# Kernel optimization log

Hardware: AMD Instinct MI355X
Metric: run time of the kernel (lower is better)

The kernel has to match this reference:

```python
import jax, jax.numpy as jnp
import numpy as np

V, D, H, L, F, S, B = 32000, 1024, 16, 6, 4096, 1024, 2
DK = D // H
SCALE = float(np.sqrt(DK))
NEG = -1e9


def _make_pe(max_len, d_model):
    pos = np.arange(max_len, dtype=np.float32)[:, None]
    div = np.exp(np.arange(0, d_model, 2, dtype=np.float32) * (-np.log(10000.0) / d_model))
    pe = np.zeros((max_len, d_model), dtype=np.float32)
    pe[:, 0::2] = np.sin(pos * div)
    pe[:, 1::2] = np.cos(pos * div)
    return jnp.asarray(pe)


def _ln(x, g, b, eps=1e-5):
    m = x.mean(-1, keepdims=True)
    v = ((x - m) ** 2).mean(-1, keepdims=True)
    return (x - m) / jnp.sqrt(v + eps) * g + b


def setup_inputs() -> dict:
    key = jax.random.key(0)
    ks = jax.random.split(key, 10)
    std = 0.02
    tokens = jax.random.randint(ks[0], (B, S), 0, V)
    emb = (jax.random.normal(ks[1], (V, D)) * std).at[0].set(0.0)  # padding_idx=0 row zeroed
    pe = _make_pe(4096, D)
    Wq = jax.random.normal(ks[2], (L, D, D)) * std
    Wk = jax.random.normal(ks[3], (L, D, D)) * std
    Wv = jax.random.normal(ks[4], (L, D, D)) * std
    Wo = jax.random.normal(ks[5], (L, D, D)) * std
    bo = jnp.zeros((L, D))
    g1 = jnp.ones((L, D)); be1 = jnp.zeros((L, D))
    g2 = jnp.ones((L, D)); be2 = jnp.zeros((L, D))
    W1 = jax.random.normal(ks[6], (L, D, F)) * std
    b1 = jnp.zeros((L, F))
    W2 = jax.random.normal(ks[7], (L, F, D)) * std
    b2 = jnp.zeros((L, D))
    gf = jnp.ones((D,)); bf = jnp.zeros((D,))
    Wout = jax.random.normal(ks[8], (D, V)) * std
    bout = jnp.zeros((V,))
    return dict(tokens=tokens, emb=emb, pe=pe, Wq=Wq, Wk=Wk, Wv=Wv, Wo=Wo, bo=bo,
                g1=g1, be1=be1, g2=g2, be2=be2, W1=W1, b1=b1, W2=W2, b2=b2,
                gf=gf, bf=bf, Wout=Wout, bout=bout)


def reference(tokens, emb, pe, Wq, Wk, Wv, Wo, bo, g1, be1, g2, be2,
              W1, b1, W2, b2, gf, bf, Wout, bout):
    Bx, Sx = tokens.shape
    x = emb[tokens] * jnp.sqrt(jnp.float32(D)) + pe[:Sx]  # (B,S,D)
    pad = tokens == 0  # (B,S) padding mask
    causal = jnp.triu(jnp.ones((Sx, Sx), dtype=bool), 1)
    mask = causal[None, None] | pad[:, None, None, :]  # (B,1,S,S), True = masked
    for l in range(L):
        h = _ln(x, g1[l], be1[l])
        q = (h @ Wq[l]).reshape(Bx, Sx, H, DK)
        k = (h @ Wk[l]).reshape(Bx, Sx, H, DK)
        v = (h @ Wv[l]).reshape(Bx, Sx, H, DK)
        scores = jnp.einsum('bqhd,bkhd->bhqk', q, k) / SCALE
        scores = jnp.where(mask, NEG, scores)  # masked_fill(mask, -1e9)
        a = jax.nn.softmax(scores, axis=-1)
        ctx = jnp.einsum('bhqk,bkhd->bqhd', a, v).reshape(Bx, Sx, D)
        x = x + ctx @ Wo[l] + bo[l]
        h = _ln(x, g2[l], be2[l])
        x = x + jax.nn.gelu(h @ W1[l] + b1[l], approximate=False) @ W2[l] + b2[l]
    x = _ln(x, gf, bf)
    return x @ Wout + bout  # (B,S,V)
```

## Files before the change

### kernel.cpp

```cpp
#include <hip/hip_runtime.h>
#include <hip/hip_bf16.h>
#include <stdint.h>

typedef __hip_bfloat16 bf16;
typedef __attribute__((ext_vector_type(8))) short bf16x8;
typedef __attribute__((ext_vector_type(4))) float f32x4;

#define DEV static __device__ __forceinline__

DEV float b2f(bf16 v) { return __bfloat162float(v); }
DEV bf16  f2b(float v) { return __float2bfloat16(v); }

DEV float u2f(unsigned short u) {
  unsigned int x = (unsigned int)u << 16;
  float f;
  __builtin_memcpy(&f, &x, 4);
  return f;
}

DEV void gload16(const void* g, void* l) {
  __builtin_amdgcn_global_load_lds(
      (__attribute__((address_space(1))) void*)(void*)g,
      (__attribute__((address_space(3))) void*)l, 16, 0, 0);
}

DEV f32x4 mfma16(bf16x8 a, bf16x8 b, f32x4 c) {
  return __builtin_amdgcn_mfma_f32_16x16x32_bf16(a, b, c, 0, 0, 0);
}

__global__ __launch_bounds__(256) void embed_kernel(
    const int* __restrict__ tok, const float* __restrict__ emb,
    const float* __restrict__ pe, float* __restrict__ x)
{
  const int r = blockIdx.x, t = threadIdx.x;
  const int s = r & 1023;
  const int tk = tok[r];
  const int d = t * 4;
  const float* ep = emb + (size_t)tk * 1024 + d;
  const float* pp = pe + (size_t)s * 1024 + d;
  float* xp = x + (size_t)r * 1024 + d;
  #pragma unroll
  for (int j = 0; j < 4; ++j)
    xp[j] = ep[j] * 32.0f + pp[j];
}

__global__ __launch_bounds__(256) void ln_kernel(
    const float* __restrict__ x, const float* __restrict__ g,
    const float* __restrict__ be, bf16* __restrict__ h)
{
  const int r = blockIdx.x, t = threadIdx.x;
  const float4 v = ((const float4*)(x + (size_t)r * 1024))[t];
  float s  = v.x + v.y + v.z + v.w;
  float sq = v.x * v.x + v.y * v.y + v.z * v.z + v.w * v.w;
  #pragma unroll
  for (int d = 1; d < 64; d <<= 1) {
    s  += __shfl_xor(s, d);
    sq += __shfl_xor(sq, d);
  }
  __shared__ float red[8];
  const int w = t >> 6, l = t & 63;
  if (l == 0) { red[w] = s; red[4 + w] = sq; }
  __syncthreads();
  s  = red[0] + red[1] + red[2] + red[3];
  sq = red[4] + red[5] + red[6] + red[7];
  const float mean = s * (1.0f / 1024.0f);
  const float var  = sq * (1.0f / 1024.0f) - mean * mean;
  const float inv  = 1.0f / sqrtf(var + 1e-5f);
  bf16* hp = h + (size_t)r * 1024 + t * 4;
  const float* gp = g + t * 4;
  const float* bp = be + t * 4;
  const float vv[4] = {v.x, v.y, v.z, v.w};
  #pragma unroll
  for (int j = 0; j < 4; ++j)
    hp[j] = f2b((vv[j] - mean) * inv * gp[j] + bp[j]);
}

__global__ __launch_bounds__(256) void ln_res_kernel(
    float* __restrict__ x, const bf16* __restrict__ P, int np,
    const float* __restrict__ bias, const float* __restrict__ g,
    const float* __restrict__ be, bf16* __restrict__ h)
{
  const int r = blockIdx.x, t = threadIdx.x;
  float4 v = ((const float4*)(x + (size_t)r * 1024))[t];
  for (int i = 0; i < np; ++i) {
    const ushort4 pv = ((const ushort4*)(P + ((size_t)i * 2048 + r) * 1024))[t];
    v.x += u2f(pv.x); v.y += u2f(pv.y); v.z += u2f(pv.z); v.w += u2f(pv.w);
  }
  const float4 bv = ((const float4*)bias)[t];
  v.x += bv.x; v.y += bv.y; v.z += bv.z; v.w += bv.w;

  float s  = v.x + v.y + v.z + v.w;
  float sq = v.x * v.x + v.y * v.y + v.z * v.z + v.w * v.w;
  #pragma unroll
  for (int d = 1; d < 64; d <<= 1) {
    s  += __shfl_xor(s, d);
    sq += __shfl_xor(sq, d);
  }
  __shared__ float red[8];
  const int w = t >> 6, l = t & 63;
  if (l == 0) { red[w] = s; red[4 + w] = sq; }
  __syncthreads();
  s  = red[0] + red[1] + red[2] + red[3];
  sq = red[4] + red[5] + red[6] + red[7];
  const float mean = s * (1.0f / 1024.0f);
  const float var  = sq * (1.0f / 1024.0f) - mean * mean;
  const float inv  = 1.0f / sqrtf(var + 1e-5f);

  ((float4*)(x + (size_t)r * 1024))[t] = v;
  bf16* hp = h + (size_t)r * 1024 + t * 4;
  const float* gp = g + t * 4;
  const float* bp = be + t * 4;
  const float vv[4] = {v.x, v.y, v.z, v.w};
  #pragma unroll
  for (int j = 0; j < 4; ++j)
    hp[j] = f2b((vv[j] - mean) * inv * gp[j] + bp[j]);
}

DEV void transpose_tile(const float* __restrict__ in, bf16* __restrict__ out,
                        int ldin, int ldout, int r0, int c0, int t)
{
  __shared__ bf16 tile[64][64];
  #pragma unroll
  for (int i = 0; i < 4; ++i) {
    const int r = i * 16 + (t >> 4), c = (t & 15) * 4;
    const float4 v = *(const float4*)&in[(size_t)(r0 + r) * ldin + c0 + c];
    tile[r][c + 0] = f2b(v.x);
    tile[r][c + 1] = f2b(v.y);
    tile[r][c + 2] = f2b(v.z);
    tile[r][c + 3] = f2b(v.w);
  }
  __syncthreads();
  #pragma unroll
  for (int i = 0; i < 2; ++i) {
    const int oc = i * 32 + (t >> 3);
    const int rr = (t & 7) * 8;
    unsigned short tmp[8] __attribute__((aligned(16)));
    #pragma unroll
    for (int j = 0; j < 8; ++j)
      tmp[j] = ((const unsigned short*)tile)[(rr + j) * 64 + oc];
    *(uint4*)&out[(size_t)(c0 + oc) * ldout + r0 + rr] = *(const uint4*)tmp;
  }
}

__global__ __launch_bounds__(256) void transpose_cast_kernel(
    const float* __restrict__ in, bf16* __restrict__ out, int ldin, int ldout)
{
  transpose_tile(in, out, ldin, ldout, blockIdx.y * 64, blockIdx.x * 64, threadIdx.x);
}

DEV void prep_dispatch(int wid,
    const float* Wq, const float* Wk, const float* Wv, const float* Wo,
    const float* W1, const float* W2,
    bf16* WqkvT, bf16* WoT, bf16* W1T, bf16* W2T, int t)
{
  const float* src; bf16* dst; int ldin, ldout, tx, ty;
  if (wid < 768) {
    const int m = wid >> 8, tt = wid & 255;
    src = (m == 0) ? Wq : (m == 1) ? Wk : Wv;
    dst = WqkvT + (size_t)m * 1024 * 1024;
    ldin = 1024; ldout = 1024; tx = tt & 15; ty = tt >> 4;
  } else if (wid < 1024) {
    const int tt = wid - 768;
    src = Wo; dst = WoT; ldin = 1024; ldout = 1024; tx = tt & 15; ty = tt >> 4;
  } else if (wid < 2048) {
    const int tt = wid - 1024;
    src = W1; dst = W1T; ldin = 4096; ldout = 1024; tx = tt & 63; ty = tt >> 6;
  } else {
    const int tt = wid - 2048;
    src = W2; dst = W2T; ldin = 1024; ldout = 4096; tx = tt & 15; ty = tt >> 4;
  }
  transpose_tile(src, dst, ldin, ldout, ty * 64, tx * 64, t);
}

__global__ __launch_bounds__(256) void prep_layer_kernel(
    const float* __restrict__ Wq, const float* __restrict__ Wk,
    const float* __restrict__ Wv, const float* __restrict__ Wo,
    const float* __restrict__ W1, const float* __restrict__ W2,
    bf16* __restrict__ WqkvT, bf16* __restrict__ WoT,
    bf16* __restrict__ W1T, bf16* __restrict__ W2T)
{
  prep_dispatch(blockIdx.x, Wq, Wk, Wv, Wo, W1, W2,
                WqkvT, WoT, W1T, W2T, threadIdx.x);
}

__global__ __launch_bounds__(256) void prep_all_kernel(
    const float* __restrict__ Wq, const float* __restrict__ Wk,
    const float* __restrict__ Wv, const float* __restrict__ Wo,
    const float* __restrict__ W1, const float* __restrict__ W2,
    bf16* __restrict__ WqkvT, bf16* __restrict__ WoT,
    bf16* __restrict__ W1T, bf16* __restrict__ W2T)
{
  const int layer = blockIdx.x / 3072;
  const int wid = blockIdx.x - layer * 3072;
  const size_t DD = (size_t)1024 * 1024, DF = (size_t)1024 * 4096;
  prep_dispatch(wid,
      Wq + layer * DD, Wk + layer * DD, Wv + layer * DD, Wo + layer * DD,
      W1 + layer * DF, W2 + layer * DF,
      WqkvT + layer * 3 * DD, WoT + layer * DD,
      W1T + layer * DF, W2T + layer * DF, threadIdx.x);
}

__global__ __launch_bounds__(256) void transpose_v_kernel(
    const bf16* __restrict__ qkv, bf16* __restrict__ vT)
{
  __shared__ bf16 tile[64][64];
  const int t = threadIdx.x;
  const int s0 = blockIdx.x * 64;
  const int bh = blockIdx.y;
  const int b = bh >> 4, h = bh & 15;
  const bf16* in = qkv + (size_t)(b * 1024) * 3072 + 2048 + h * 64;
  #pragma unroll
  for (int i = 0; i < 2; ++i) {
    const int r = i * 32 + (t >> 3), c = (t & 7) * 8;
    *(uint4*)&tile[r][c] = *(const uint4*)&in[(size_t)(s0 + r) * 3072 + c];
  }
  __syncthreads();
  bf16* out = vT + (size_t)(bh * 64) * 1024;
  #pragma unroll
  for (int i = 0; i < 2; ++i) {
    const int oc = i * 32 + (t >> 3);
    const int rr = (t & 7) * 8;
    unsigned short tmp[8] __attribute__((aligned(16)));
    #pragma unroll
    for (int j = 0; j < 8; ++j)
      tmp[j] = ((const unsigned short*)tile)[(rr + j) * 64 + oc];
    *(uint4*)&out[(size_t)oc * 1024 + s0 + rr] = *(const uint4*)tmp;
  }
}

template<int EPI, int BM, int SWZ>
__global__ __launch_bounds__(256) void gemm_pl(
    const bf16* __restrict__ A, int lda,
    const bf16* __restrict__ BT, int ldb,
    void* __restrict__ Cp, int ldc,
    const float* __restrict__ bias,
    int ksl)
{
  constexpr int ABUF = BM * 32;
  constexpr int MR = BM / 32;
  __shared__ bf16 As[3 * ABUF];
  __shared__ bf16 Bs[3 * 4096];
  const int t = threadIdx.x;

  int bm, bn;
  if constexpr (SWZ) {
    const int nbm = gridDim.x;
    const int nwg = nbm * gridDim.y;
    int wid = blockIdx.x + nbm * blockIdx.y;
    wid = (wid & 7) * (nwg >> 3) + (wid >> 3);
    bm = wid % nbm; bn = wid / nbm;
  } else {
    bm = blockIdx.x; bn = blockIdx.y;
  }

  const int w = t >> 6, l = t & 63;
  const int wr = (w >> 1) * (BM / 2), wc = (w & 1) * 64;
  const int l15 = l & 15, l4 = l >> 4;
  const int kbeg = blockIdx.z * ksl;
  const int ntiles = ksl >> 5;

  const int colblk = (((t & 3) ^ ((t >> 3) & 3))) * 8;
  const bf16* gA = A  + (size_t)(bm * BM  + (t >> 2)) * lda + colblk + kbeg;
  const bf16* gB = BT + (size_t)(bn * 128 + (t >> 2)) * ldb + colblk + kbeg;
  bf16* lA = As + w * 512;
  bf16* lB = Bs + w * 512;

  auto stage = [&](int tile, int buf) {
    const int k0 = tile * 32;
    gload16(gA + k0, lA + buf * ABUF);
    if constexpr (BM == 128)
      gload16(gA + (size_t)64 * lda + k0, lA + buf * ABUF + 2048);
    gload16(gB + k0, lB + buf * 4096);
    gload16(gB + (size_t)64 * ldb + k0, lB + buf * 4096 + 2048);
  };

  f32x4 acc[MR][4];
  #pragma unroll
  for (int m = 0; m < MR; ++m)
    #pragma unroll
    for (int n = 0; n < 4; ++n)
      acc[m][n] = (f32x4){0.f, 0.f, 0.f, 0.f};

  stage(0, 0);
  stage(1, 1);

  const int rdcol = ((l4 ^ ((l15 >> 1) & 3))) * 8;

  int buf = 0;
  for (int kt = 0; kt < ntiles; ++kt) {
    if (kt + 2 < ntiles) {
      int pb = buf + 2; if (pb >= 3) pb -= 3;
      stage(kt + 2, pb);
      __builtin_amdgcn_sched_barrier(0);
      if constexpr (BM == 128) asm volatile("s_waitcnt vmcnt(8)" ::: "memory");
      else                     asm volatile("s_waitcnt vmcnt(6)" ::: "memory");
    } else if (kt + 1 < ntiles) {
      if constexpr (BM == 128) asm volatile("s_waitcnt vmcnt(4)" ::: "memory");
      else                     asm volatile("s_waitcnt vmcnt(3)" ::: "memory");
    } else {
      asm volatile("s_waitcnt vmcnt(0)" ::: "memory");
    }
    __builtin_amdgcn_s_barrier();
    __builtin_amdgcn_sched_barrier(0);

    const bf16* Ab = As + buf * ABUF;
    const bf16* Bb = Bs + buf * 4096;
    bf16x8 af[MR], bfr[4];
    #pragma unroll
    for (int m = 0; m < MR; ++m)
      af[m] = *(const bf16x8*)&Ab[(wr + m * 16 + l15) * 32 + rdcol];
    #pragma unroll
    for (int n = 0; n < 4; ++n)
      bfr[n] = *(const bf16x8*)&Bb[(wc + n * 16 + l15) * 32 + rdcol];
    #pragma unroll
    for (int m = 0; m < MR; ++m)
      #pragma unroll
      for (int n = 0; n < 4; ++n)
        acc[m][n] = mfma16(af[m], bfr[n], acc[m][n]);

    __builtin_amdgcn_sched_barrier(0);
    __builtin_amdgcn_s_barrier();
    if (++buf >= 3) buf = 0;
  }

  const int crow = bm * BM + wr, ccol = bn * 128 + wc;
  #pragma unroll
  for (int n = 0; n < 4; ++n) {
    const int col = ccol + n * 16 + l15;
    float bv = 0.f;
    if (EPI == 1 || EPI == 2) bv = bias[col];
    #pragma unroll
    for (int m = 0; m < MR; ++m) {
      const int row = crow + m * 16 + l4 * 4;
      #pragma unroll
      for (int r = 0; r < 4; ++r) {
        const float v = acc[m][n][r];
        if (EPI == 0) {
          ((bf16*)Cp)[(size_t)(row + r) * ldc + col] = f2b(v);
        } else if (EPI == 1) {
          ((float*)Cp)[(size_t)(row + r) * ldc + col] = v + bv;
        } else if (EPI == 2) {
          const float u = v + bv;
          const float gel = 0.5f * u * (1.0f + erff(u * 0.70710678118654752f));
          ((bf16*)Cp)[(size_t)(row + r) * ldc + col] = f2b(gel);
        } else {
          const int M = gridDim.x * BM;
          ((bf16*)Cp)[((size_t)blockIdx.z * M + row + r) * ldc + col] = f2b(v);
        }
      }
    }
  }
}

__global__ __launch_bounds__(512, 2) void gemm256(
    const bf16* __restrict__ A, int lda,
    const bf16* __restrict__ BT, int ldb,
    float* __restrict__ C, int ldc,
    const float* __restrict__ bias, int K)
{
  __shared__ bf16 As[3][8192];
  __shared__ bf16 Bs[3][8192];
  const int t = threadIdx.x;

  const int nbm = gridDim.x;
  const int nwg = nbm * gridDim.y;
  int wid = blockIdx.x + nbm * blockIdx.y;
  wid = (wid & 7) * (nwg >> 3) + (wid >> 3);
  const int bm = wid % nbm, bn = wid / nbm;

  const int w = t >> 6, l = t & 63;
  const int wm = w >> 2, wn = w & 3;
  const int l15 = l & 15, l4 = l >> 4;

  const int colblk = ((t & 3) ^ ((t >> 3) & 3)) * 8;
  const bf16* gA = A  + (size_t)(bm * 256 + (t >> 2)) * lda + colblk;
  const bf16* gB = BT + (size_t)(bn * 256 + (t >> 2)) * ldb + colblk;
  const int dst = w * 512;

  const int rd = (l4 ^ ((l15 >> 1) & 3)) * 8;
  const int arow = wm * 128 + l15;
  const int brow = wn * 64 + l15;

  f32x4 acc[8][4];
  #pragma unroll
  for (int m = 0; m < 8; ++m)
    #pragma unroll
    for (int n = 0; n < 4; ++n)
      acc[m][n] = (f32x4){0.f, 0.f, 0.f, 0.f};

  const int NT = K >> 5;

  auto stageA = [&](int kt, int buf) {
    const int k0 = kt * 32;
    gload16(gA + k0, &As[buf][dst]);
    gload16(gA + (size_t)128 * lda + k0, &As[buf][4096 + dst]);
  };
  auto stageB = [&](int kt, int buf) {
    const int k0 = kt * 32;
    gload16(gB + k0, &Bs[buf][dst]);
    gload16(gB + (size_t)128 * ldb + k0, &Bs[buf][4096 + dst]);
  };

  stageA(0, 0); stageB(0, 0);
  stageA(1, 1); stageB(1, 1);

  int buf = 0;
  for (int kt = 0; kt < NT; ++kt) {
    if (kt + 1 < NT) asm volatile("s_waitcnt vmcnt(4)" ::: "memory");
    else             asm volatile("s_waitcnt vmcnt(0)" ::: "memory");
    __builtin_amdgcn_s_barrier();
    __builtin_amdgcn_sched_barrier(0);

    int pb = buf + 2; if (pb >= 3) pb -= 3;
    const bf16* Ab = As[buf];
    const bf16* Bb = Bs[buf];

    bf16x8 bfr[4], af[4];
    #pragma unroll
    for (int n = 0; n < 4; ++n)
      bfr[n] = *(const bf16x8*)&Bb[(brow + n * 16) * 32 + rd];
    #pragma unroll
    for (int m = 0; m < 4; ++m)
      af[m] = *(const bf16x8*)&Ab[(arow + m * 16) * 32 + rd];
    if (kt + 2 < NT) stageA(kt + 2, pb);
    asm volatile("s_waitcnt lgkmcnt(0)" ::: "memory");
    __builtin_amdgcn_sched_barrier(0);
    __builtin_amdgcn_s_setprio(1);
    #pragma unroll
    for (int m = 0; m < 4; ++m)
      #pragma unroll
      for (int n = 0; n < 4; ++n)
        acc[m][n] = mfma16(af[m], bfr[n], acc[m][n]);
    __builtin_amdgcn_s_setprio(0);
    __builtin_amdgcn_sched_barrier(0);
    __builtin_amdgcn_s_barrier();

    #pragma unroll
    for (int m = 0; m < 4; ++m)
      af[m] = *(const bf16x8*)&Ab[(arow + (m + 4) * 16) * 32 + rd];
    if (kt + 2 < NT) stageB(kt + 2, pb);
    asm volatile("s_waitcnt lgkmcnt(0)" ::: "memory");
    __builtin_amdgcn_sched_barrier(0);
    __builtin_amdgcn_s_setprio(1);
    #pragma unroll
    for (int m = 0; m < 4; ++m)
      #pragma unroll
      for (int n = 0; n < 4; ++n)
        acc[m + 4][n] = mfma16(af[m], bfr[n], acc[m + 4][n]);
    __builtin_amdgcn_s_setprio(0);
    __builtin_amdgcn_sched_barrier(0);
    __builtin_amdgcn_s_barrier();

    if (++buf >= 3) buf = 0;
  }

  #pragma unroll
  for (int n = 0; n < 4; ++n) {
    const int col = bn * 256 + wn * 64 + n * 16 + l15;
    const float bv = bias[col];
    #pragma unroll
    for (int m = 0; m < 8; ++m) {
      const int row = bm * 256 + wm * 128 + m * 16 + l4 * 4;
      #pragma unroll
      for (int r = 0; r < 4; ++r)
        C[(size_t)(row + r) * ldc + col] = acc[m][n][r] + bv;
    }
  }
}

__global__ __launch_bounds__(512) void attn_kernel(
    const bf16* __restrict__ qkv, const bf16* __restrict__ vT,
    const int* __restrict__ tokens, bf16* __restrict__ ctx)
{
  __shared__ bf16 Ks[128 * 64];
  __shared__ bf16 VTs[64 * 128];
  __shared__ bf16 Ps[128 * 128];

  const int qt = blockIdx.x;
  const int bh = blockIdx.y;
  const int b = bh >> 4, h = bh & 15;
  const int t = threadIdx.x, w = t >> 6, l = t & 63;
  const int l15 = l & 15, l4 = l >> 4;
  const int q0 = qt * 128;

  bf16x8 aq[2];
  #pragma unroll
  for (int ks = 0; ks < 2; ++ks)
    aq[ks] = *(const bf16x8*)(qkv +
        (size_t)(b * 1024 + q0 + w * 16 + l15) * 3072 +
        h * 64 + ks * 32 + l4 * 8);

  f32x4 o[4];
  float m_run[4], l_run[4];
  #pragma unroll
  for (int r = 0; r < 4; ++r) { m_run[r] = -1e30f; l_run[r] = 0.f; }
  #pragma unroll
  for (int nn = 0; nn < 4; ++nn)
    o[nn] = (f32x4){0.f, 0.f, 0.f, 0.f};

  const bf16* kb = qkv + (size_t)(b * 1024) * 3072 + 1024 + h * 64;
  const bf16* vb = vT + (size_t)(bh * 64) * 1024;
  const int* tb = tokens + b * 1024;

  const int kSrcCol = ((t & 7) ^ ((t >> 3) & 7)) * 8;
  const int vSrcCol = ((t & 15) ^ ((t >> 4) & 15)) * 8;

  for (int jt = 0; jt <= qt; ++jt) {
    const int j0 = jt * 128;
    __syncthreads();
    #pragma unroll
    for (int i = 0; i < 2; ++i)
      gload16(kb + (size_t)(j0 + i * 64 + (t >> 3)) * 3072 + kSrcCol,
              Ks + i * 4096 + w * 512);
    #pragma unroll
    for (int i = 0; i < 2; ++i)
      gload16(vb + (size_t)(i * 32 + (t >> 4)) * 1024 + j0 + vSrcCol,
              VTs + i * 4096 + w * 512);
    __syncthreads();

    f32x4 s[8];
    #pragma unroll
    for (int n = 0; n < 8; ++n)
      s[n] = (f32x4){0.f, 0.f, 0.f, 0.f};
    #pragma unroll
    for (int ks = 0; ks < 2; ++ks) {
      #pragma unroll
      for (int n = 0; n < 8; ++n) {
        const bf16x8 bk = *(const bf16x8*)
            &Ks[(n * 16 + l15) * 64 + ((ks * 32 + l4 * 8) ^ ((l15 & 7) * 8))];
        s[n] = mfma16(aq[ks], bk, s[n]);
      }
    }

    float padv[8];
    #pragma unroll
    for (int n = 0; n < 8; ++n)
      padv[n] = (tb[j0 + n * 16 + l15] == 0) ? 1.f : 0.f;

    #pragma unroll
    for (int r = 0; r < 4; ++r) {
      const int rloc = l4 * 4 + r;
      const int qrow = q0 + w * 16 + rloc;
      float vals[8];
      float mx = -1e30f;
      #pragma unroll
      for (int n = 0; n < 8; ++n) {
        const int jg = j0 + n * 16 + l15;
        float v = s[n][r] * 0.125f;
        if (jg > qrow || padv[n] != 0.f) v = -1e9f;
        vals[n] = v;
        mx = fmaxf(mx, v);
      }
      #pragma unroll
      for (int d = 1; d < 16; d <<= 1) mx = fmaxf(mx, __shfl_xor(mx, d));
      const float newm = fmaxf(m_run[r], mx);
      const float sc = __expf(m_run[r] - newm);
      m_run[r] = newm;
      float rs = 0.f;
      #pragma unroll
      for (int n = 0; n < 8; ++n) {
        const float pv = __expf(vals[n] - newm);
        vals[n] = pv;
        rs += pv;
      }
      #pragma unroll
      for (int d = 1; d < 16; d <<= 1) rs += __shfl_xor(rs, d);
      l_run[r] = l_run[r] * sc + rs;
      #pragma unroll
      for (int nn = 0; nn < 4; ++nn) o[nn][r] = o[nn][r] * sc;
      #pragma unroll
      for (int n = 0; n < 8; ++n)
        Ps[(w * 16 + rloc) * 128 + ((n * 16 + l15) ^ (rloc * 8))] = f2b(vals[n]);
    }
    asm volatile("s_waitcnt lgkmcnt(0)" ::: "memory");

    #pragma unroll
    for (int ks = 0; ks < 4; ++ks) {
      const bf16x8 ap = *(const bf16x8*)
          &Ps[(w * 16 + l15) * 128 + ((ks * 32 + l4 * 8) ^ (l15 * 8))];
      #pragma unroll
      for (int nn = 0; nn < 4; ++nn) {
        const bf16x8 bv = *(const bf16x8*)
            &VTs[(nn * 16 + l15) * 128 + ((ks * 32 + l4 * 8) ^ (l15 * 8))];
        o[nn] = mfma16(ap, bv, o[nn]);
      }
    }
  }

  #pragma unroll
  for (int r = 0; r < 4; ++r) {
    const float inv = 1.0f / l_run[r];
    const int qrow = q0 + w * 16 + l4 * 4 + r;
    #pragma unroll
    for (int nn = 0; nn < 4; ++nn)
      ctx[(size_t)(b * 1024 + qrow) * 1024 + h * 64 + nn * 16 + l15] =
          f2b(o[nn][r] * inv);
  }
}

__global__ __launch_bounds__(64) void attn_fixup_kernel(
    const int* __restrict__ tokens, const bf16* __restrict__ vT,
    bf16* __restrict__ ctx)
{
  const int bh = blockIdx.x;
  const int b = bh >> 4, h = bh & 15;
  __shared__ int p0s;
  if (threadIdx.x == 0) {
    int p = 0;
    const int* tb = tokens + b * 1024;
    while (p < 1024 && tb[p] == 0) ++p;
    p0s = p;
  }
  __syncthreads();
  const int P0 = p0s;
  if (P0 == 0) return;
  const int dk = threadIdx.x;
  const bf16* vrow = vT + (size_t)(bh * 64 + dk) * 1024;
  float sum = 0.f;
  for (int sIdx = 0; sIdx < 1024; ++sIdx) sum += b2f(vrow[sIdx]);
  const bf16 mv = f2b(sum * (1.0f / 1024.0f));
  for (int q = 0; q < P0; ++q)
    ctx[(size_t)(b * 1024 + q) * 1024 + h * 64 + dk] = mv;
}

extern "C" void kernel_launch(void* const* d_in, const int* in_sizes, int n_in,
                              void* d_out, int out_size, void* d_ws, size_t ws_size,
                              hipStream_t stream)
{
  (void)in_sizes; (void)n_in; (void)out_size;
  const int*   tokens = (const int*)d_in[0];
  const float* emb  = (const float*)d_in[1];
  const float* pe   = (const float*)d_in[2];
  const float* Wq   = (const float*)d_in[3];
  const float* Wk   = (const float*)d_in[4];
  const float* Wv   = (const float*)d_in[5];
  const float* Wo   = (const float*)d_in[6];
  const float* bo   = (const float*)d_in[7];
  const float* g1   = (const float*)d_in[8];
  const float* be1  = (const float*)d_in[9];
  const float* g2   = (const float*)d_in[10];
  const float* be2  = (const float*)d_in[11];
  const float* W1   = (const float*)d_in[12];
  const float* b1   = (const float*)d_in[13];
  const float* W2   = (const float*)d_in[14];
  const float* b2   = (const float*)d_in[15];
  const float* gf   = (const float*)d_in[16];
  const float* bff  = (const float*)d_in[17];
  const float* Wout = (const float*)d_in[18];
  const float* bout = (const float*)d_in[19];
  float* out = (float*)d_out;

  char* p = (char*)d_ws;
  auto alloc = [&](size_t bytes) {
    char* q = p;
    p += (bytes + 255) & ~(size_t)255;
    return q;
  };
  float* x    = (float*)alloc((size_t)2048 * 1024 * 4);
  bf16* Pp    = (bf16*)alloc((size_t)4 * 2048 * 1024 * 2);
  bf16* h     = (bf16*)alloc((size_t)2048 * 1024 * 2);
  bf16* qkv   = (bf16*)alloc((size_t)2048 * 3072 * 2);
  bf16* vT    = (bf16*)alloc((size_t)2048 * 1024 * 2);
  bf16* ctx   = (bf16*)alloc((size_t)2048 * 1024 * 2);
  bf16* ff    = (bf16*)alloc((size_t)2048 * 4096 * 2);
  bf16* WoutT = (bf16*)alloc((size_t)32000 * 1024 * 2);

  const size_t DD = (size_t)1024 * 1024;
  const size_t DF = (size_t)1024 * 4096;

  const size_t perLayerW = (3 * DD + DD + DF + DF) * 2;
  const size_t used = (size_t)(p - (char*)d_ws);
  const bool fullprep = ws_size >= used + 6 * perLayerW + 8192;
  const int NL = fullprep ? 6 : 1;
  bf16* WqkvT = (bf16*)alloc((size_t)NL * 3 * DD * 2);
  bf16* WoT   = (bf16*)alloc((size_t)NL * DD * 2);
  bf16* W1T   = (bf16*)alloc((size_t)NL * DF * 2);
  bf16* W2T   = (bf16*)alloc((size_t)NL * DF * 2);

  if (fullprep)
    prep_all_kernel<<<6 * 3072, 256, 0, stream>>>(
        Wq, Wk, Wv, Wo, W1, W2, WqkvT, WoT, W1T, W2T);

  embed_kernel<<<2048, 256, 0, stream>>>(tokens, emb, pe, x);

  for (int l = 0; l < 6; ++l) {
    const bf16* wqkvt; const bf16* wot; const bf16* w1t; const bf16* w2t;
    if (fullprep) {
      wqkvt = WqkvT + (size_t)l * 3 * DD;
      wot   = WoT   + (size_t)l * DD;
      w1t   = W1T   + (size_t)l * DF;
      w2t   = W2T   + (size_t)l * DF;
    } else {
      prep_layer_kernel<<<3072, 256, 0, stream>>>(
          Wq + l * DD, Wk + l * DD, Wv + l * DD, Wo + l * DD,
          W1 + l * DF, W2 + l * DF, WqkvT, WoT, W1T, W2T);
      wqkvt = WqkvT; wot = WoT; w1t = W1T; w2t = W2T;
    }

    if (l == 0)
      ln_kernel<<<2048, 256, 0, stream>>>(x, g1, be1, h);
    else
      ln_res_kernel<<<2048, 256, 0, stream>>>(
          x, Pp, 4, b2 + (l - 1) * 1024, g1 + l * 1024, be1 + l * 1024, h);

    gemm_pl<0, 128, 0><<<dim3(16, 24, 1), 256, 0, stream>>>(
        h, 1024, wqkvt, 1024, qkv, 3072, (const float*)nullptr, 1024);
    transpose_v_kernel<<<dim3(16, 32), 256, 0, stream>>>(qkv, vT);
    attn_kernel<<<dim3(8, 32), 512, 0, stream>>>(qkv, vT, tokens, ctx);
    attn_fixup_kernel<<<32, 64, 0, stream>>>(tokens, vT, ctx);
    gemm_pl<3, 128, 0><<<dim3(16, 8, 4), 256, 0, stream>>>(
        ctx, 1024, wot, 1024, Pp, 1024, (const float*)nullptr, 256);
    ln_res_kernel<<<2048, 256, 0, stream>>>(
        x, Pp, 4, bo + l * 1024, g2 + l * 1024, be2 + l * 1024, h);
    gemm_pl<2, 128, 0><<<dim3(16, 32, 1), 256, 0, stream>>>(
        h, 1024, w1t, 1024, ff, 4096, b1 + l * 4096, 1024);
    gemm_pl<3, 128, 0><<<dim3(16, 8, 4), 256, 0, stream>>>(
        ff, 4096, w2t, 4096, Pp, 1024, (const float*)nullptr, 1024);
  }

  ln_res_kernel<<<2048, 256, 0, stream>>>(x, Pp, 4, b2 + 5 * 1024, gf, bff, h);
  transpose_cast_kernel<<<dim3(500, 16), 256, 0, stream>>>(Wout, WoutT, 32000, 1024);
  gemm256<<<dim3(8, 125), 512, 0, stream>>>(
      h, 1024, WoutT, 1024, out, 32000, bout, 1024);
}
```

Baseline: 1.347 ms.

## Pipeline GEMM in K-pairs with four buffers and fuse V transpose into QKV epilogue

The per-layer GEMM kernel now processes two 32-wide K tiles per iteration using four LDS buffers. It reads all fragments before the barrier, issues the next prefetch, then runs 32 MFMAs under raised wave priority, so there are fewer barriers per K step. The separate V-transpose kernel is removed: the QKV GEMM epilogue writes the V columns directly in transposed layout into vT, saving a launch and a read/write pass. The cost is more LDS per block (64 KB), which may lower occupancy, and scattered 8-byte transposed stores.

```diff
diff --git a/kernel.cpp b/kernel.cpp
--- a/kernel.cpp
+++ b/kernel.cpp
@@ -16,6 +16,13 @@
   float f;
   __builtin_memcpy(&f, &x, 4);
   return f;
+}
+
+DEV unsigned short f2u(float v) {
+  bf16 b = f2b(v);
+  unsigned short u;
+  __builtin_memcpy(&u, &b, 2);
+  return u;
 }
 
 DEV void gload16(const void* g, void* l) {
@@ -200,46 +207,17 @@
       W1T + layer * DF, W2T + layer * DF, threadIdx.x);
 }
 
-__global__ __launch_bounds__(256) void transpose_v_kernel(
-    const bf16* __restrict__ qkv, bf16* __restrict__ vT)
-{
-  __shared__ bf16 tile[64][64];
-  const int t = threadIdx.x;
-  const int s0 = blockIdx.x * 64;
-  const int bh = blockIdx.y;
-  const int b = bh >> 4, h = bh & 15;
-  const bf16* in = qkv + (size_t)(b * 1024) * 3072 + 2048 + h * 64;
-  #pragma unroll
-  for (int i = 0; i < 2; ++i) {
-    const int r = i * 32 + (t >> 3), c = (t & 7) * 8;
-    *(uint4*)&tile[r][c] = *(const uint4*)&in[(size_t)(s0 + r) * 3072 + c];
-  }
-  __syncthreads();
-  bf16* out = vT + (size_t)(bh * 64) * 1024;
-  #pragma unroll
-  for (int i = 0; i < 2; ++i) {
-    const int oc = i * 32 + (t >> 3);
-    const int rr = (t & 7) * 8;
-    unsigned short tmp[8] __attribute__((aligned(16)));
-    #pragma unroll
-    for (int j = 0; j < 8; ++j)
-      tmp[j] = ((const unsigned short*)tile)[(rr + j) * 64 + oc];
-    *(uint4*)&out[(size_t)oc * 1024 + s0 + rr] = *(const uint4*)tmp;
-  }
-}
-
-template<int EPI, int BM, int SWZ>
+template<int EPI, int SWZ>
 __global__ __launch_bounds__(256) void gemm_pl(
     const bf16* __restrict__ A, int lda,
     const bf16* __restrict__ BT, int ldb,
     void* __restrict__ Cp, int ldc,
     const float* __restrict__ bias,
+    bf16* __restrict__ vTp,
     int ksl)
 {
-  constexpr int ABUF = BM * 32;
-  constexpr int MR = BM / 32;
-  __shared__ bf16 As[3 * ABUF];
-  __shared__ bf16 Bs[3 * 4096];
+  __shared__ bf16 As[4][4096];
+  __shared__ bf16 Bs[4][4096];
   const int t = threadIdx.x;
 
   int bm, bn;
@@ -254,88 +232,102 @@
   }
 
   const int w = t >> 6, l = t & 63;
-  const int wr = (w >> 1) * (BM / 2), wc = (w & 1) * 64;
+  const int wr = (w >> 1) * 64, wc = (w & 1) * 64;
   const int l15 = l & 15, l4 = l >> 4;
   const int kbeg = blockIdx.z * ksl;
-  const int ntiles = ksl >> 5;
+  const int npairs = ksl >> 6;
 
   const int colblk = (((t & 3) ^ ((t >> 3) & 3))) * 8;
-  const bf16* gA = A  + (size_t)(bm * BM  + (t >> 2)) * lda + colblk + kbeg;
+  const bf16* gA = A  + (size_t)(bm * 128 + (t >> 2)) * lda + colblk + kbeg;
   const bf16* gB = BT + (size_t)(bn * 128 + (t >> 2)) * ldb + colblk + kbeg;
-  bf16* lA = As + w * 512;
-  bf16* lB = Bs + w * 512;
+  const int dst = w * 512;
 
   auto stage = [&](int tile, int buf) {
     const int k0 = tile * 32;
-    gload16(gA + k0, lA + buf * ABUF);
-    if constexpr (BM == 128)
-      gload16(gA + (size_t)64 * lda + k0, lA + buf * ABUF + 2048);
-    gload16(gB + k0, lB + buf * 4096);
-    gload16(gB + (size_t)64 * ldb + k0, lB + buf * 4096 + 2048);
+    gload16(gA + k0, &As[buf][dst]);
+    gload16(gA + (size_t)64 * lda + k0, &As[buf][2048 + dst]);
+    gload16(gB + k0, &Bs[buf][dst]);
+    gload16(gB + (size_t)64 * ldb + k0, &Bs[buf][2048 + dst]);
   };
 
-  f32x4 acc[MR][4];
-  #pragma unroll
-  for (int m = 0; m < MR; ++m)
+  f32x4 acc[4][4];
+  #pragma unroll
+  for (int m = 0; m < 4; ++m)
     #pragma unroll
     for (int n = 0; n < 4; ++n)
       acc[m][n] = (f32x4){0.f, 0.f, 0.f, 0.f};
 
-  stage(0, 0);
-  stage(1, 1);
+  stage(0, 0); stage(1, 1);
+  stage(2, 2); stage(3, 3);
 
   const int rdcol = ((l4 ^ ((l15 >> 1) & 3))) * 8;
 
-  int buf = 0;
-  for (int kt = 0; kt < ntiles; ++kt) {
-    if (kt + 2 < ntiles) {
-      int pb = buf + 2; if (pb >= 3) pb -= 3;
-      stage(kt + 2, pb);
-      __builtin_amdgcn_sched_barrier(0);
-      if constexpr (BM == 128) asm volatile("s_waitcnt vmcnt(8)" ::: "memory");
-      else                     asm volatile("s_waitcnt vmcnt(6)" ::: "memory");
-    } else if (kt + 1 < ntiles) {
-      if constexpr (BM == 128) asm volatile("s_waitcnt vmcnt(4)" ::: "memory");
-      else                     asm volatile("s_waitcnt vmcnt(3)" ::: "memory");
-    } else {
-      asm volatile("s_waitcnt vmcnt(0)" ::: "memory");
-    }
+  for (int pp = 0; pp < npairs; ++pp) {
+    const int base = (pp & 1) << 1;
+    if (pp + 1 < npairs) asm volatile("s_waitcnt vmcnt(8)" ::: "memory");
+    else                 asm volatile("s_waitcnt vmcnt(0)" ::: "memory");
     __builtin_amdgcn_s_barrier();
     __builtin_amdgcn_sched_barrier(0);
 
-    const bf16* Ab = As + buf * ABUF;
-    const bf16* Bb = Bs + buf * 4096;
-    bf16x8 af[MR], bfr[4];
-    #pragma unroll
-    for (int m = 0; m < MR; ++m)
-      af[m] = *(const bf16x8*)&Ab[(wr + m * 16 + l15) * 32 + rdcol];
+    bf16x8 af0[4], bf0[4], af1[4], bf1[4];
+    #pragma unroll
+    for (int m = 0; m < 4; ++m)
+      af0[m] = *(const bf16x8*)&As[base][(wr + m * 16 + l15) * 32 + rdcol];
     #pragma unroll
     for (int n = 0; n < 4; ++n)
-      bfr[n] = *(const bf16x8*)&Bb[(wc + n * 16 + l15) * 32 + rdcol];
-    #pragma unroll
-    for (int m = 0; m < MR; ++m)
-      #pragma unroll
-      for (int n = 0; n < 4; ++n)
-        acc[m][n] = mfma16(af[m], bfr[n], acc[m][n]);
-
+      bf0[n] = *(const bf16x8*)&Bs[base][(wc + n * 16 + l15) * 32 + rdcol];
+    #pragma unroll
+    for (int m = 0; m < 4; ++m)
+      af1[m] = *(const bf16x8*)&As[base + 1][(wr + m * 16 + l15) * 32 + rdcol];
+    #pragma unroll
+    for (int n = 0; n < 4; ++n)
+      bf1[n] = *(const bf16x8*)&Bs[base + 1][(wc + n * 16 + l15) * 32 + rdcol];
+    asm volatile("s_waitcnt lgkmcnt(0)" ::: "memory");
     __builtin_amdgcn_sched_barrier(0);
     __builtin_amdgcn_s_barrier();
-    if (++buf >= 3) buf = 0;
-  }
-
-  const int crow = bm * BM + wr, ccol = bn * 128 + wc;
+
+    if (pp + 2 < npairs) {
+      stage(2 * pp + 4, base);
+      stage(2 * pp + 5, base + 1);
+    }
+
+    __builtin_amdgcn_s_setprio(1);
+    #pragma unroll
+    for (int m = 0; m < 4; ++m)
+      #pragma unroll
+      for (int n = 0; n < 4; ++n)
+        acc[m][n] = mfma16(af0[m], bf0[n], acc[m][n]);
+    #pragma unroll
+    for (int m = 0; m < 4; ++m)
+      #pragma unroll
+      for (int n = 0; n < 4; ++n)
+        acc[m][n] = mfma16(af1[m], bf1[n], acc[m][n]);
+    __builtin_amdgcn_s_setprio(0);
+    __builtin_amdgcn_sched_barrier(0);
+  }
+
+  const int crow = bm * 128 + wr, ccol = bn * 128 + wc;
   #pragma unroll
   for (int n = 0; n < 4; ++n) {
     const int col = ccol + n * 16 + l15;
     float bv = 0.f;
     if (EPI == 1 || EPI == 2) bv = bias[col];
     #pragma unroll
-    for (int m = 0; m < MR; ++m) {
+    for (int m = 0; m < 4; ++m) {
       const int row = crow + m * 16 + l4 * 4;
+      if (EPI == 4 && ccol >= 2048) {
+        const int b = row >> 10, s = row & 1023;
+        const int hk = col - 2048;
+        ushort4 pk;
+        pk.x = f2u(acc[m][n][0]); pk.y = f2u(acc[m][n][1]);
+        pk.z = f2u(acc[m][n][2]); pk.w = f2u(acc[m][n][3]);
+        *(ushort4*)&vTp[((size_t)b * 1024 + hk) * 1024 + s] = pk;
+        continue;
+      }
       #pragma unroll
       for (int r = 0; r < 4; ++r) {
         const float v = acc[m][n][r];
-        if (EPI == 0) {
+        if (EPI == 0 || EPI == 4) {
           ((bf16*)Cp)[(size_t)(row + r) * ldc + col] = f2b(v);
         } else if (EPI == 1) {
           ((float*)Cp)[(size_t)(row + r) * ldc + col] = v + bv;
@@ -344,7 +336,7 @@
           const float gel = 0.5f * u * (1.0f + erff(u * 0.70710678118654752f));
           ((bf16*)Cp)[(size_t)(row + r) * ldc + col] = f2b(gel);
         } else {
-          const int M = gridDim.x * BM;
+          const int M = gridDim.x * 128;
           ((bf16*)Cp)[((size_t)blockIdx.z * M + row + r) * ldc + col] = f2b(v);
         }
       }
@@ -703,19 +695,20 @@
       ln_res_kernel<<<2048, 256, 0, stream>>>(
           x, Pp, 4, b2 + (l - 1) * 1024, g1 + l * 1024, be1 + l * 1024, h);
 
-    gemm_pl<0, 128, 0><<<dim3(16, 24, 1), 256, 0, stream>>>(
-        h, 1024, wqkvt, 1024, qkv, 3072, (const float*)nullptr, 1024);
-    transpose_v_kernel<<<dim3(16, 32), 256, 0, stream>>>(qkv, vT);
+    gemm_pl<4, 0><<<dim3(16, 24, 1), 256, 0, stream>>>(
+        h, 1024, wqkvt, 1024, qkv, 3072, (const float*)nullptr, vT, 1024);
     attn_kernel<<<dim3(8, 32), 512, 0, stream>>>(qkv, vT, tokens, ctx);
     attn_fixup_kernel<<<32, 64, 0, stream>>>(tokens, vT, ctx);
-    gemm_pl<3, 128, 0><<<dim3(16, 8, 4), 256, 0, stream>>>(
-        ctx, 1024, wot, 1024, Pp, 1024, (const float*)nullptr, 256);
+    gemm_pl<3, 0><<<dim3(16, 8, 4), 256, 0, stream>>>(
+        ctx, 1024, wot, 1024, Pp, 1024, (const float*)nullptr,
+        (bf16*)nullptr, 256);
     ln_res_kernel<<<2048, 256, 0, stream>>>(
         x, Pp, 4, bo + l * 1024, g2 + l * 1024, be2 + l * 1024, h);
-    gemm_pl<2, 128, 0><<<dim3(16, 32, 1), 256, 0, stream>>>(
-        h, 1024, w1t, 1024, ff, 4096, b1 + l * 4096, 1024);
-    gemm_pl<3, 128, 0><<<dim3(16, 8, 4), 256, 0, stream>>>(
-        ff, 4096, w2t, 4096, Pp, 1024, (const float*)nullptr, 1024);
+    gemm_pl<2, 0><<<dim3(16, 32, 1), 256, 0, stream>>>(
+        h, 1024, w1t, 1024, ff, 4096, b1 + l * 4096, (bf16*)nullptr, 1024);
+    gemm_pl<3, 0><<<dim3(16, 8, 4), 256, 0, stream>>>(
+        ff, 4096, w2t, 4096, Pp, 1024, (const float*)nullptr,
+        (bf16*)nullptr, 1024);
   }
 
   ln_res_kernel<<<2048, 256, 0, stream>>>(x, Pp, 4, b2 + 5 * 1024, gf, bff, h);
```

After: 1.252 ms. 1.08x faster.
